# Performance work log

Measured on AMD Instinct MI355X. Metric: run time of the kernel, lower is better.

The kernel has to match this reference:

```python
import jax, jax.numpy as jnp
import numpy as np

B, N, C_IN, C_OUT, K = 8, 4096, 64, 128, 15
RADIUS = 0.1            # 2.5 * grid_size(0.04) * sigma(1.0)
MAX_NN = 34
KP_EXTENT = 0.04        # point_influence = prev_grid_size * sigma
KERNEL_RADIUS = 1.5 * KP_EXTENT
NEG_SLOPE = 0.2
BN_EPS = 1e-5


def setup_inputs() -> dict:
    key = jax.random.key(0)
    k1, k2, k3, k4 = jax.random.split(key, 4)
    xyz = jax.random.uniform(k1, (B, N, 3), dtype=jnp.float32)
    feats = jax.random.normal(k2, (B, N, C_IN), dtype=jnp.float32)
    # fixed kernel point disposition inside the kernel ball (requires_grad=False in torch)
    kp = jax.random.normal(k3, (K, 3), dtype=jnp.float32)
    kp = kp / (jnp.linalg.norm(kp, axis=-1, keepdims=True) + 1e-6) * KERNEL_RADIUS * 0.7
    kp = kp.at[0].set(0.0)  # center point
    std = float(np.sqrt(2.0 / (K * C_IN)))
    weight = jax.random.normal(k4, (K, C_IN, C_OUT), dtype=jnp.float32) * std
    gamma = jnp.ones((C_OUT,), dtype=jnp.float32)
    beta = jnp.zeros((C_OUT,), dtype=jnp.float32)
    return {"xyz": xyz, "feats": feats, "K_points": kp, "weight": weight,
            "gamma": gamma, "beta": beta}


def _ball_query(xyz):
    # xyz: [B, N, 3] -> flat neighbor idx [B*N, MAX_NN] into the concatenated
    # point array; missing neighbors get shadow index B*N.
    b_, n_, _ = xyz.shape
    shadow = b_ * n_

    def per_cloud(pts, b):
        d2 = jnp.sum((pts[:, None, :] - pts[None, :, :]) ** 2, axis=-1)  # [N, N]
        neg_d2, idx = jax.lax.top_k(-d2, MAX_NN)                         # k nearest
        valid = (-neg_d2) <= RADIUS ** 2
        return jnp.where(valid, idx + b * n_, shadow)

    return jax.vmap(per_cloud)(xyz, jnp.arange(b_)).reshape(b_ * n_, MAX_NN)


def _kpconv_block(xyz, feats, K_points, weight, gamma, beta):
    b_, n_, _ = xyz.shape
    pts = xyz.reshape(b_ * n_, 3)
    f = feats.reshape(b_ * n_, C_IN)
    nidx = _ball_query(xyz)                                   # [M, nn]
    # shadow point far away / zero features (KPConv_ops)
    pts_pad = jnp.concatenate([pts, jnp.full((1, 3), 1e6, pts.dtype)], axis=0)
    f_pad = jnp.concatenate([f, jnp.zeros((1, C_IN), f.dtype)], axis=0)
    nbr = pts_pad[nidx] - pts[:, None, :]                     # [M, nn, 3] relative coords
    sq = jnp.sum((nbr[:, :, None, :] - K_points) ** 2, -1)    # [M, nn, K]
    w = jnp.maximum(1.0 - jnp.sqrt(sq) / KP_EXTENT, 0.0)      # linear influence
    nf = f_pad[nidx]                                          # [M, nn, Cin]
    wf = jnp.einsum('mnk,mnc->mkc', w, nf)                    # per-kernel-point feats
    out = jnp.einsum('mkc,kcd->md', wf, weight)               # [M, Cout]
    # FastBatchNorm1d (training-mode batch stats, biased var) + LeakyReLU
    mu = out.mean(axis=0)
    var = out.var(axis=0)
    out = (out - mu) * jax.lax.rsqrt(var + BN_EPS) * gamma + beta
    out = jnp.where(out >= 0, out, NEG_SLOPE * out)
    return out.reshape(b_, n_, C_OUT)


def reference(xyz, feats, K_points, weight, gamma, beta):
    return _kpconv_block(xyz, feats, K_points, weight, gamma, beta)
```

## Files before the change

kernel.cpp:

```cpp
#include <hip/hip_runtime.h>


#define NB     8
#define NPTS   4096
#define M_TOT  32768
#define CIN    64
#define COUT   128
#define NKP    15
#define NCELL  1728
#define UCAP   400
#define R2EFF  (0.082f * 0.082f)
#define KP_INV 25.0f
#define NEG_SLOPE 0.2f
#define KCP    960
#define WFROW  1920
#define SP     40

typedef float f32x4_t __attribute__((ext_vector_type(4)));
typedef short bf16x8_t __attribute__((ext_vector_type(8)));

__device__ __forceinline__ unsigned short f2bf(float f) {
  union { float f; unsigned u; } v; v.f = f;
  unsigned r = v.u + 0x7FFF + ((v.u >> 16) & 1);
  return (unsigned short)(r >> 16);
}
__device__ __forceinline__ unsigned short f2bf_fast(float f) {
  union { float f; unsigned u; } v; v.f = f;
  return (unsigned short)((v.u + 0x8000u) >> 16);
}
__device__ __forceinline__ int cell_of(float x, float y, float z) {
  int cx = (int)(x * 12.f); cx = cx > 11 ? 11 : cx;
  int cy = (int)(y * 12.f); cy = cy > 11 ? 11 : cy;
  int cz = (int)(z * 12.f); cz = cz > 11 ? 11 : cz;
  return (cz * 12 + cy) * 12 + cx;
}

__global__ __launch_bounds__(256) void k0a_hist(
    const float* __restrict__ xyz, int* __restrict__ cellcnt)
{
  const int pt = blockIdx.x * 256 + threadIdx.x;
  const float x = xyz[pt * 3], y = xyz[pt * 3 + 1], z = xyz[pt * 3 + 2];
  const int b = pt >> 12;
  atomicAdd(&cellcnt[b * NCELL + cell_of(x, y, z)], 1);
}

__global__ __launch_bounds__(256) void k0b_scan_kWF(
    const int* __restrict__ cellcnt, int* __restrict__ cellstart,
    const float* __restrict__ W, unsigned short* __restrict__ WtF)
{
  if (blockIdx.x >= 8) {
    const int idx = (blockIdx.x - 8) * 256 + threadIdx.x;
    const int L  = idx & 63;
    const int g  = idx >> 6;
    const int kk = g % 30;
    const int ct = g / 30;
    const int d  = ct * 16 + (L & 15);
    const int kcb = (L >> 4) * 8 + kk * 32;
    union { unsigned short s[8]; uint4 v; } u;
    #pragma unroll
    for (int e = 0; e < 8; e++) {
      const int kc = kcb + e;
      const int k  = kc >> 6;
      const int c  = kc & 63;
      u.s[e] = f2bf(W[(size_t)k * (CIN * COUT) + c * COUT + d]);
    }
    *(uint4*)&WtF[(size_t)idx * 8] = u.v;
    return;
  }
  __shared__ int ps[256];
  const int b = blockIdx.x, t = threadIdx.x;
  int local[7], s = 0;
  #pragma unroll
  for (int i = 0; i < 7; i++) {
    const int cid = t * 7 + i;
    const int c = (cid < NCELL) ? cellcnt[b * NCELL + cid] : 0;
    local[i] = c; s += c;
  }
  ps[t] = s; __syncthreads();
  for (int off = 1; off < 256; off <<= 1) {
    int v = (t >= off) ? ps[t - off] : 0;
    __syncthreads();
    ps[t] += v;
    __syncthreads();
  }
  int run = ps[t] - s;
  #pragma unroll
  for (int i = 0; i < 7; i++) {
    const int cid = t * 7 + i;
    if (cid < NCELL) { cellstart[b * 1729 + cid] = run; run += local[i]; }
  }
  if (t == 255) cellstart[b * 1729 + NCELL] = ps[255];
}

__global__ __launch_bounds__(256) void k0b_old(
    const int* __restrict__ cellcnt, int* __restrict__ cellstart,
    const float* __restrict__ W, unsigned short* __restrict__ Wt)
{
  if (blockIdx.x >= 8) {
    const int idx = (blockIdx.x - 8) * 256 + threadIdx.x;
    const int c = idx & 63, d = idx >> 6;
    #pragma unroll
    for (int k = 0; k < NKP; k++)
      Wt[(size_t)d * KCP + k * 64 + c] =
          f2bf(W[(size_t)k * (CIN * COUT) + c * COUT + d]);
    return;
  }
  __shared__ int ps[256];
  const int b = blockIdx.x, t = threadIdx.x;
  int local[7], s = 0;
  #pragma unroll
  for (int i = 0; i < 7; i++) {
    const int cid = t * 7 + i;
    const int c = (cid < NCELL) ? cellcnt[b * NCELL + cid] : 0;
    local[i] = c; s += c;
  }
  ps[t] = s; __syncthreads();
  for (int off = 1; off < 256; off <<= 1) {
    int v = (t >= off) ? ps[t - off] : 0;
    __syncthreads();
    ps[t] += v;
    __syncthreads();
  }
  int run = ps[t] - s;
  #pragma unroll
  for (int i = 0; i < 7; i++) {
    const int cid = t * 7 + i;
    if (cid < NCELL) { cellstart[b * 1729 + cid] = run; run += local[i]; }
  }
  if (t == 255) cellstart[b * 1729 + NCELL] = ps[255];
}

__global__ __launch_bounds__(256) void k0c_scatter(
    const float* __restrict__ xyz, const float* __restrict__ feats,
    const int* __restrict__ cellstart, int* __restrict__ cellfill,
    int* __restrict__ qorder, float4* __restrict__ xyzs,
    unsigned short* __restrict__ fsorted)
{
  const int pt = blockIdx.x * 256 + threadIdx.x;
  const float x = xyz[pt * 3], y = xyz[pt * 3 + 1], z = xyz[pt * 3 + 2];
  const int b = pt >> 12;
  const int cid = cell_of(x, y, z);
  const int slot = atomicAdd(&cellfill[b * NCELL + cid], 1);
  const int pos = b * NPTS + cellstart[b * 1729 + cid] + slot;
  qorder[pos] = pt;
  xyzs[pos] = make_float4(x, y, z, 0.f);
  const float* src = &feats[(size_t)pt * CIN];
  uint4* dst = (uint4*)&fsorted[(size_t)pos * CIN];
  #pragma unroll
  for (int g = 0; g < 8; g++) {
    float4 a = *(const float4*)(src + g * 8);
    float4 c = *(const float4*)(src + g * 8 + 4);
    union { unsigned short s[8]; uint4 v; } u;
    u.s[0] = f2bf(a.x); u.s[1] = f2bf(a.y); u.s[2] = f2bf(a.z); u.s[3] = f2bf(a.w);
    u.s[4] = f2bf(c.x); u.s[5] = f2bf(c.y); u.s[6] = f2bf(c.z); u.s[7] = f2bf(c.w);
    dst[g] = u.v;
  }
}

__global__ __launch_bounds__(256, 5) void k2a_conv(
    const float4* __restrict__ xyzs, const unsigned short* __restrict__ fsorted,
    const float* __restrict__ kpts, const int* __restrict__ cellstart,
    unsigned short* __restrict__ wfg)
{
  __shared__ char smraw[32000] __attribute__((aligned(16)));
  float4*         Pu   = (float4*)smraw;
  unsigned short* cpos = (unsigned short*)(smraw + 6400);
  short (*S)[SP]       = (short(*)[SP])(smraw + 6400);
  short (*FT)[SP]      = (short(*)[SP])(smraw + 26880);

  __shared__ float4 qd[16];
  __shared__ float  kp[NKP][4];
  __shared__ int    Tsh;
  __shared__ int    ucnt;

  const int tid = threadIdx.x;
  const int w   = tid >> 6;
  const int L   = tid & 63;
  const int m0  = blockIdx.x * 16;
  const int b   = m0 >> 12;

  if (tid >= 64 && tid < 64 + NKP) {
    const int k = tid - 64;
    const float kx = kpts[k * 3], ky = kpts[k * 3 + 1], kz = kpts[k * 3 + 2];
    kp[k][0] = -2.f * kx; kp[k][1] = -2.f * ky; kp[k][2] = -2.f * kz;
    kp[k][3] = kx * kx + ky * ky + kz * kz;
  }

  if (tid < 64) {
    int cxm = 12, cym = 12, czm = 12, cxM = -1, cyM = -1, czM = -1;
    if (tid < 16) {
      const float4 Q = xyzs[m0 + tid];
      qd[tid] = Q;
      int a = (int)(Q.x * 12.f); a = a > 11 ? 11 : a;
      int c = (int)(Q.y * 12.f); c = c > 11 ? 11 : c;
      int d = (int)(Q.z * 12.f); d = d > 11 ? 11 : d;
      cxm = cxM = a; cym = cyM = c; czm = czM = d;
    }
    #pragma unroll
    for (int off = 8; off >= 1; off >>= 1) {
      int v;
      v = __shfl_xor(cxm, off); cxm = v < cxm ? v : cxm;
      v = __shfl_xor(cxM, off); cxM = v > cxM ? v : cxM;
      v = __shfl_xor(cym, off); cym = v < cym ? v : cym;
      v = __shfl_xor(cyM, off); cyM = v > cyM ? v : cyM;
      v = __shfl_xor(czm, off); czm = v < czm ? v : czm;
      v = __shfl_xor(czM, off); czM = v > czM ? v : czM;
    }
    cxm = __shfl(cxm, 0); cxM = __shfl(cxM, 0);
    cym = __shfl(cym, 0); cyM = __shfl(cyM, 0);
    czm = __shfl(czm, 0); czM = __shfl(czM, 0);

    const int x0 = cxm > 0 ? cxm - 1 : 0, x1 = cxM < 11 ? cxM + 1 : 11;
    const int y0 = cym > 0 ? cym - 1 : 0, y1 = cyM < 11 ? cyM + 1 : 11;
    const int z0 = czm > 0 ? czm - 1 : 0, z1 = czM < 11 ? czM + 1 : 11;
    const int yspan = y1 - y0 + 1;
    int nr = yspan * (z1 - z0 + 1);
    nr = nr > 64 ? 64 : nr;

    int rs = 0, len = 0;
    if (tid < nr) {
      const int zz = z0 + tid / yspan, yy = y0 + tid % yspan;
      const int base = b * 1729 + (zz * 12 + yy) * 12;
      rs  = cellstart[base + x0];
      len = cellstart[base + x1 + 1] - rs;
    }
    int incl = len;
    #pragma unroll
    for (int off = 1; off < 64; off <<= 1) {
      const int v = __shfl_up(incl, off);
      if (tid >= off) incl += v;
    }
    const int excl = incl - len;
    for (int i = 0; i < len; i++) cpos[excl + i] = (unsigned short)(rs + i);
    if (tid == 63) Tsh = incl;
    if (tid == 62) ucnt = 0;
  }
  __syncthreads();
  const int T = Tsh;

  for (int tb = 0; tb < T; tb += 256) {
    const int t = tb + tid;
    if (t < T) {
      const int pos = (int)cpos[t];
      const float4 P = xyzs[b * NPTS + pos];
      float best = 1e9f;
      #pragma unroll
      for (int i = 0; i < 16; i++) {
        const float4 Q = qd[i];
        const float dx = P.x - Q.x, dy = P.y - Q.y, dz = P.z - Q.z;
        const float d2 = dx * dx + dy * dy + dz * dz;
        best = d2 < best ? d2 : best;
      }
      if (best <= R2EFF) {
        const int slot = atomicAdd(&ucnt, 1);
        if (slot < UCAP)
          Pu[slot] = make_float4(P.x, P.y, P.z, __int_as_float(pos));
      }
    }
  }
  __syncthreads();
  int U = ucnt; U = U > UCAP ? UCAP : U;

  const int ln = L & 15;
  const int kh = L >> 4;
  const int qh = tid >> 5;
  const int nn = tid & 31;

  f32x4_t acc[16];
  #pragma unroll
  for (int mt = 0; mt < 16; mt++) acc[mt] = (f32x4_t){0.f, 0.f, 0.f, 0.f};

  for (int ub = 0; ub < U; ub += 32) {
    {
      const int c  = tid & 63;
      const int i0 = tid >> 6;
      #pragma unroll
      for (int ii = 0; ii < 8; ii++) {
        const int i = ii * 4 + i0;
        const int u = ub + i;
        short v = 0;
        if (u < U) {
          const int pos = __float_as_int(Pu[u].w);
          v = (short)fsorted[(size_t)(b * NPTS + pos) * CIN + c];
        }
        FT[c][i] = v;
      }
    }

    bf16x8_t bb;
    #pragma unroll
    for (int half = 0; half < 2; half++) {
      {
        const int u = ub + nn;
        if (u < U) {
          const float4 P = Pu[u];
          const float4 Q = qd[half * 8 + qh];
          const float rx = P.x - Q.x, ry = P.y - Q.y, rz = P.z - Q.z;
          const float rr = rx * rx + ry * ry + rz * rz;
          #pragma unroll
          for (int k = 0; k < NKP; k++) {
            float d2 = fmaf(kp[k][0], rx,
                       fmaf(kp[k][1], ry,
                       fmaf(kp[k][2], rz, rr + kp[k][3])));
            d2 = fmaxf(d2, 0.f);
            const float wv =
                fmaxf(fmaf(-KP_INV, __builtin_amdgcn_sqrtf(d2), 1.f), 0.f);
            S[qh * 16 + k][nn] = (short)f2bf_fast(wv);
          }
          S[qh * 16 + 15][nn] = 0;
        } else {
          #pragma unroll
          for (int k = 0; k < 16; k++) S[qh * 16 + k][nn] = 0;
        }
      }
      __syncthreads();
      if (half == 0) bb = *(const bf16x8_t*)&FT[w * 16 + ln][kh * 8];
      #pragma unroll
      for (int mt = 0; mt < 8; mt++) {
        bf16x8_t aa = *(const bf16x8_t*)&S[mt * 16 + ln][kh * 8];
        acc[half * 8 + mt] =
            __builtin_amdgcn_mfma_f32_16x16x32_bf16(aa, bb, acc[half * 8 + mt],
                                                    0, 0, 0);
      }
      __syncthreads();
    }
  }

  #pragma unroll
  for (int mt = 0; mt < 16; mt++) {
    const size_t rb = (size_t)(m0 + mt) * KCP + (w * 16 + ln);
    #pragma unroll
    for (int j = 0; j < 4; j++) {
      const int k = kh * 4 + j;
      if (k < 15)
        wfg[rb + k * 64] = f2bf_fast(acc[mt][j]);
    }
  }
}

__global__ __launch_bounds__(256, 5) void k2b_gemm(
    const unsigned short* __restrict__ wfg,
    const unsigned short* __restrict__ WtF,
    const int* __restrict__ qorder, float* __restrict__ out,
    float* __restrict__ psum, float* __restrict__ psumsq)
{
  __shared__ char smraw[30720] __attribute__((aligned(16)));
  __shared__ int qm[16];

  const int tid = threadIdx.x;
  const int w   = tid >> 6;
  const int L   = tid & 63;
  const int m0  = blockIdx.x * 16;

  if (tid < 16) qm[tid] = qorder[m0 + tid];

  {
    const int r0 = tid >> 7;
    const int ch = tid & 127;
    if (ch < 120) {
      #pragma unroll
      for (int it = 0; it < 8; it++) {
        const int r = it * 2 + r0;
        const uint4 v = *(const uint4*)(wfg + (size_t)(m0 + r) * KCP + ch * 8);
        *(uint4*)(smraw + ((r * WFROW + ch * 16) ^ ((r & 7) << 4))) = v;
      }
    }
  }
  __syncthreads();

  const int ln = L & 15;
  const int kh = L >> 4;
  const int colbase = w * 32;

  f32x4_t acc2[2];
  acc2[0] = (f32x4_t){0.f, 0.f, 0.f, 0.f};
  acc2[1] = (f32x4_t){0.f, 0.f, 0.f, 0.f};

  const unsigned short* Bp = WtF + ((size_t)(w * 2 * 30) * 64 + L) * 8;
  const char* wfb = (const char*)smraw + ln * WFROW;
  const int   sw  = (ln & 7) << 4;

  #pragma unroll 6
  for (int kk = 0; kk < 30; kk++) {
    const int inr = (kh * 16 + kk * 64) ^ sw;
    bf16x8_t b0 = *(const bf16x8_t*)(Bp + kk * 512);
    bf16x8_t b1 = *(const bf16x8_t*)(Bp + 15360 + kk * 512);
    bf16x8_t a0 = *(const bf16x8_t*)(wfb + inr);
    acc2[0] = __builtin_amdgcn_mfma_f32_16x16x32_bf16(a0, b0, acc2[0], 0, 0, 0);
    acc2[1] = __builtin_amdgcn_mfma_f32_16x16x32_bf16(a0, b1, acc2[1], 0, 0, 0);
  }

  float s0 = 0.f, q0 = 0.f, s1 = 0.f, q1 = 0.f;
  #pragma unroll
  for (int j = 0; j < 4; j++) {
    s0 += acc2[0][j]; q0 += acc2[0][j] * acc2[0][j];
    s1 += acc2[1][j]; q1 += acc2[1][j] * acc2[1][j];
  }
  s0 += __shfl_xor(s0, 16); s0 += __shfl_xor(s0, 32);
  q0 += __shfl_xor(q0, 16); q0 += __shfl_xor(q0, 32);
  s1 += __shfl_xor(s1, 16); s1 += __shfl_xor(s1, 32);
  q1 += __shfl_xor(q1, 16); q1 += __shfl_xor(q1, 32);
  if (kh == 0) {
    atomicAdd(&psum[colbase + ln], s0);
    atomicAdd(&psumsq[colbase + ln], q0);
    atomicAdd(&psum[colbase + 16 + ln], s1);
    atomicAdd(&psumsq[colbase + 16 + ln], q1);
  }

  #pragma unroll
  for (int c = 0; c < 2; c++) {
    #pragma unroll
    for (int j = 0; j < 4; j++) {
      const int row = kh * 4 + j;
      out[(size_t)qm[row] * COUT + colbase + c * 16 + ln] = acc2[c][j];
    }
  }
}

__global__ __launch_bounds__(256, 5) void k2_old(
    const float4* __restrict__ xyzs, const unsigned short* __restrict__ fsorted,
    const float* __restrict__ kpts, const int* __restrict__ cellstart,
    const int* __restrict__ qorder, const unsigned short* __restrict__ Wt,
    float* __restrict__ out, float* __restrict__ psum,
    float* __restrict__ psumsq)
{
  __shared__ char smraw[32000] __attribute__((aligned(16)));
  float4*         Pu   = (float4*)smraw;
  unsigned short* cpos = (unsigned short*)(smraw + 6400);
  short (*S)[SP]       = (short(*)[SP])(smraw + 6400);
  short (*FT)[SP]      = (short(*)[SP])(smraw + 26880);

  __shared__ float4 qd[16];
  __shared__ int    qm[16];
  __shared__ float  kp[NKP][4];
  __shared__ int    Tsh;
  __shared__ int    ucnt;

  const int tid = threadIdx.x;
  const int w   = tid >> 6;
  const int L   = tid & 63;
  const int m0  = blockIdx.x * 16;
  const int b   = m0 >> 12;

  if (tid >= 64 && tid < 64 + NKP) {
    const int k = tid - 64;
    const float kx = kpts[k * 3], ky = kpts[k * 3 + 1], kz = kpts[k * 3 + 2];
    kp[k][0] = -2.f * kx; kp[k][1] = -2.f * ky; kp[k][2] = -2.f * kz;
    kp[k][3] = kx * kx + ky * ky + kz * kz;
  }

  if (tid < 64) {
    int cxm = 12, cym = 12, czm = 12, cxM = -1, cyM = -1, czM = -1;
    if (tid < 16) {
      const float4 Q = xyzs[m0 + tid];
      qd[tid] = Q;
      qm[tid] = qorder[m0 + tid];
      int a = (int)(Q.x * 12.f); a = a > 11 ? 11 : a;
      int c = (int)(Q.y * 12.f); c = c > 11 ? 11 : c;
      int d = (int)(Q.z * 12.f); d = d > 11 ? 11 : d;
      cxm = cxM = a; cym = cyM = c; czm = czM = d;
    }
    #pragma unroll
    for (int off = 8; off >= 1; off >>= 1) {
      int v;
      v = __shfl_xor(cxm, off); cxm = v < cxm ? v : cxm;
      v = __shfl_xor(cxM, off); cxM = v > cxM ? v : cxM;
      v = __shfl_xor(cym, off); cym = v < cym ? v : cym;
      v = __shfl_xor(cyM, off); cyM = v > cyM ? v : cyM;
      v = __shfl_xor(czm, off); czm = v < czm ? v : czm;
      v = __shfl_xor(czM, off); czM = v > czM ? v : czM;
    }
    cxm = __shfl(cxm, 0); cxM = __shfl(cxM, 0);
    cym = __shfl(cym, 0); cyM = __shfl(cyM, 0);
    czm = __shfl(czm, 0); czM = __shfl(czM, 0);

    const int x0 = cxm > 0 ? cxm - 1 : 0, x1 = cxM < 11 ? cxM + 1 : 11;
    const int y0 = cym > 0 ? cym - 1 : 0, y1 = cyM < 11 ? cyM + 1 : 11;
    const int z0 = czm > 0 ? czm - 1 : 0, z1 = czM < 11 ? czM + 1 : 11;
    const int yspan = y1 - y0 + 1;
    int nr = yspan * (z1 - z0 + 1);
    nr = nr > 64 ? 64 : nr;

    int rs = 0, len = 0;
    if (tid < nr) {
      const int zz = z0 + tid / yspan, yy = y0 + tid % yspan;
      const int base = b * 1729 + (zz * 12 + yy) * 12;
      rs  = cellstart[base + x0];
      len = cellstart[base + x1 + 1] - rs;
    }
    int incl = len;
    #pragma unroll
    for (int off = 1; off < 64; off <<= 1) {
      const int v = __shfl_up(incl, off);
      if (tid >= off) incl += v;
    }
    const int excl = incl - len;
    for (int i = 0; i < len; i++) cpos[excl + i] = (unsigned short)(rs + i);
    if (tid == 63) Tsh = incl;
    if (tid == 62) ucnt = 0;
  }
  __syncthreads();
  const int T = Tsh;

  for (int tb = 0; tb < T; tb += 256) {
    const int t = tb + tid;
    if (t < T) {
      const int pos = (int)cpos[t];
      const float4 P = xyzs[b * NPTS + pos];
      float best = 1e9f;
      #pragma unroll
      for (int i = 0; i < 16; i++) {
        const float4 Q = qd[i];
        const float dx = P.x - Q.x, dy = P.y - Q.y, dz = P.z - Q.z;
        const float d2 = dx * dx + dy * dy + dz * dz;
        best = d2 < best ? d2 : best;
      }
      if (best <= R2EFF) {
        const int slot = atomicAdd(&ucnt, 1);
        if (slot < UCAP)
          Pu[slot] = make_float4(P.x, P.y, P.z, __int_as_float(pos));
      }
    }
  }
  __syncthreads();
  int U = ucnt; U = U > UCAP ? UCAP : U;

  const int ln = L & 15;
  const int kh = L >> 4;
  const int qh = tid >> 5;
  const int nn = tid & 31;

  f32x4_t acc[16];
  #pragma unroll
  for (int mt = 0; mt < 16; mt++) acc[mt] = (f32x4_t){0.f, 0.f, 0.f, 0.f};

  for (int ub = 0; ub < U; ub += 32) {
    {
      const int c  = tid & 63;
      const int i0 = tid >> 6;
      #pragma unroll
      for (int ii = 0; ii < 8; ii++) {
        const int i = ii * 4 + i0;
        const int u = ub + i;
        short v = 0;
        if (u < U) {
          const int pos = __float_as_int(Pu[u].w);
          v = (short)fsorted[(size_t)(b * NPTS + pos) * CIN + c];
        }
        FT[c][i] = v;
      }
    }
    bf16x8_t bb;
    #pragma unroll
    for (int half = 0; half < 2; half++) {
      {
        const int u = ub + nn;
        if (u < U) {
          const float4 P = Pu[u];
          const float4 Q = qd[half * 8 + qh];
          const float rx = P.x - Q.x, ry = P.y - Q.y, rz = P.z - Q.z;
          const float rr = rx * rx + ry * ry + rz * rz;
          #pragma unroll
          for (int k = 0; k < NKP; k++) {
            float d2 = fmaf(kp[k][0], rx,
                       fmaf(kp[k][1], ry,
                       fmaf(kp[k][2], rz, rr + kp[k][3])));
            d2 = fmaxf(d2, 0.f);
            const float wv =
                fmaxf(fmaf(-KP_INV, __builtin_amdgcn_sqrtf(d2), 1.f), 0.f);
            S[qh * 16 + k][nn] = (short)f2bf_fast(wv);
          }
          S[qh * 16 + 15][nn] = 0;
        } else {
          #pragma unroll
          for (int k = 0; k < 16; k++) S[qh * 16 + k][nn] = 0;
        }
      }
      __syncthreads();
      if (half == 0) bb = *(const bf16x8_t*)&FT[w * 16 + ln][kh * 8];
      #pragma unroll
      for (int mt = 0; mt < 8; mt++) {
        bf16x8_t aa = *(const bf16x8_t*)&S[mt * 16 + ln][kh * 8];
        acc[half * 8 + mt] =
            __builtin_amdgcn_mfma_f32_16x16x32_bf16(aa, bb, acc[half * 8 + mt],
                                                    0, 0, 0);
      }
      __syncthreads();
    }
  }

  {
    const int c = w * 16 + ln;
    #pragma unroll
    for (int mt = 0; mt < 16; mt++) {
      #pragma unroll
      for (int j = 0; j < 4; j++) {
        const int k = kh * 4 + j;
        if (k < 15) {
          const int byteo = (mt * WFROW + ((k * 64 + c) << 1)) ^ ((mt & 7) << 4);
          *(unsigned short*)(smraw + byteo) = f2bf_fast(acc[mt][j]);
        }
      }
    }
  }
  __syncthreads();

  const int colbase = w * 32;
  f32x4_t acc2[2];
  acc2[0] = (f32x4_t){0.f, 0.f, 0.f, 0.f};
  acc2[1] = (f32x4_t){0.f, 0.f, 0.f, 0.f};

  const unsigned short* Bp0 = &Wt[(size_t)(colbase + ln) * KCP + kh * 8];
  const unsigned short* Bp1 = Bp0 + 16 * KCP;
  const char* wfb = (const char*)smraw + ln * WFROW;
  const int   sw  = (ln & 7) << 4;

  #pragma unroll 6
  for (int kk = 0; kk < 30; kk++) {
    const int ko  = kk * 32;
    const int inr = (kh * 16 + kk * 64) ^ sw;
    bf16x8_t b0 = *(const bf16x8_t*)(Bp0 + ko);
    bf16x8_t b1 = *(const bf16x8_t*)(Bp1 + ko);
    bf16x8_t a0 = *(const bf16x8_t*)(wfb + inr);
    acc2[0] = __builtin_amdgcn_mfma_f32_16x16x32_bf16(a0, b0, acc2[0], 0, 0, 0);
    acc2[1] = __builtin_amdgcn_mfma_f32_16x16x32_bf16(a0, b1, acc2[1], 0, 0, 0);
  }

  float s0 = 0.f, q0 = 0.f, s1 = 0.f, q1 = 0.f;
  #pragma unroll
  for (int j = 0; j < 4; j++) {
    s0 += acc2[0][j]; q0 += acc2[0][j] * acc2[0][j];
    s1 += acc2[1][j]; q1 += acc2[1][j] * acc2[1][j];
  }
  s0 += __shfl_xor(s0, 16); s0 += __shfl_xor(s0, 32);
  q0 += __shfl_xor(q0, 16); q0 += __shfl_xor(q0, 32);
  s1 += __shfl_xor(s1, 16); s1 += __shfl_xor(s1, 32);
  q1 += __shfl_xor(q1, 16); q1 += __shfl_xor(q1, 32);
  if (kh == 0) {
    atomicAdd(&psum[colbase + ln], s0);
    atomicAdd(&psumsq[colbase + ln], q0);
    atomicAdd(&psum[colbase + 16 + ln], s1);
    atomicAdd(&psumsq[colbase + 16 + ln], q1);
  }

  #pragma unroll
  for (int c = 0; c < 2; c++) {
    #pragma unroll
    for (int j = 0; j < 4; j++) {
      const int row = kh * 4 + j;
      out[(size_t)qm[row] * COUT + colbase + c * 16 + ln] = acc2[c][j];
    }
  }
}

__global__ __launch_bounds__(256) void k4_norm(
    float* __restrict__ out, const float* __restrict__ psum,
    const float* __restrict__ psumsq, const float* __restrict__ gamma,
    const float* __restrict__ beta)
{
  __shared__ float a_s[128], b_s[128];
  if (threadIdx.x < 128) {
    const int d = threadIdx.x;
    double mu  = (double)psum[d] / (double)M_TOT;
    double var = (double)psumsq[d] / (double)M_TOT - mu * mu;
    float rstd = (float)(1.0 / sqrt(var + 1e-5));
    float a = rstd * gamma[d];
    a_s[d] = a;
    b_s[d] = beta[d] - (float)mu * a;
  }
  __syncthreads();
  const int idx = blockIdx.x * 256 + threadIdx.x;
  float4 v = ((const float4*)out)[idx];
  const int d0 = (idx * 4) & 127;
  float y0 = v.x * a_s[d0 + 0] + b_s[d0 + 0];
  float y1 = v.y * a_s[d0 + 1] + b_s[d0 + 1];
  float y2 = v.z * a_s[d0 + 2] + b_s[d0 + 2];
  float y3 = v.w * a_s[d0 + 3] + b_s[d0 + 3];
  v.x = y0 >= 0.f ? y0 : NEG_SLOPE * y0;
  v.y = y1 >= 0.f ? y1 : NEG_SLOPE * y1;
  v.z = y2 >= 0.f ? y2 : NEG_SLOPE * y2;
  v.w = y3 >= 0.f ? y3 : NEG_SLOPE * y3;
  ((float4*)out)[idx] = v;
}

extern "C" void kernel_launch(void* const* d_in, const int* in_sizes, int n_in,
                              void* d_out, int out_size, void* d_ws,
                              size_t ws_size, hipStream_t stream)
{
  const float* xyz   = (const float*)d_in[0];
  const float* feats = (const float*)d_in[1];
  const float* kpts  = (const float*)d_in[2];
  const float* W     = (const float*)d_in[3];
  const float* gamma = (const float*)d_in[4];
  const float* beta  = (const float*)d_in[5];
  float* out = (float*)d_out;

  char* ws = (char*)d_ws;
  int*            cellcnt   = (int*)(ws + 0);
  int*            cellfill  = (int*)(ws + 55296);
  float*          psum      = (float*)(ws + 110592);
  float*          psumsq    = (float*)(ws + 111104);
  int*            cellstart = (int*)(ws + 111616);
  int*            qorder    = (int*)(ws + 167040);
  float4*         xyzs      = (float4*)(ws + 298112);
  unsigned short* fsorted   = (unsigned short*)(ws + 822400);
  unsigned short* Wtbuf     = (unsigned short*)(ws + 5016704);
  unsigned short* wfg       = (unsigned short*)(ws + 5262464);

  const size_t NEED = 5262464ull + 62914560ull;

  hipMemsetAsync(ws, 0, 111616, stream);

  if (ws_size >= NEED) {
    k0a_hist    <<< 128, 256, 0, stream>>>(xyz, cellcnt);
    k0b_scan_kWF<<<  68, 256, 0, stream>>>(cellcnt, cellstart, W, Wtbuf);
    k0c_scatter <<< 128, 256, 0, stream>>>(xyz, feats, cellstart, cellfill,
                                           qorder, xyzs, fsorted);
    k2a_conv    <<<2048, 256, 0, stream>>>(xyzs, fsorted, kpts, cellstart,
                                           wfg);
    k2b_gemm    <<<2048, 256, 0, stream>>>(wfg, Wtbuf, qorder, out,
                                           psum, psumsq);
    k4_norm     <<<(out_size / 4) / 256, 256, 0, stream>>>(out, psum, psumsq,
                                                           gamma, beta);
  } else {
    k0a_hist    <<< 128, 256, 0, stream>>>(xyz, cellcnt);
    k0b_old     <<<  40, 256, 0, stream>>>(cellcnt, cellstart, W, Wtbuf);
    k0c_scatter <<< 128, 256, 0, stream>>>(xyz, feats, cellstart, cellfill,
                                           qorder, xyzs, fsorted);
    k2_old      <<<2048, 256, 0, stream>>>(xyzs, fsorted, kpts, cellstart,
                                           qorder, Wtbuf, out, psum, psumsq);
    k4_norm     <<<(out_size / 4) / 256, 256, 0, stream>>>(out, psum, psumsq,
                                                           gamma, beta);
  }
}
```

Before: 205.3 us.

## Retile GEMM stage to 128x128 blocks with double-buffered direct-to-LDS loads

The second-stage GEMM moves from 16-row blocks, which read a pre-swizzled weight layout straight from global memory, to 128x128 output tiles. Each of 4 waves computes a 64x64 sub-tile, and A/B k-slices are staged into swizzled LDS through global_load_lds with double buffering. The weight prep goes back to the plain [d][k*64+c] transpose kernel. This raises reuse of weight and activation tiles per block, but leaves only 256 blocks with fewer waves per CU and more accumulator registers.

New measurement: 174.2 us. -15.1%, faster.

```diff
diff --git a/kernel.cpp b/kernel.cpp
--- a/kernel.cpp
+++ b/kernel.cpp
@@ -34,6 +34,11 @@
   int cz = (int)(z * 12.f); cz = cz > 11 ? 11 : cz;
   return (cz * 12 + cy) * 12 + cx;
 }
+__device__ __forceinline__ void gld_lds16(const unsigned short* g, void* l) {
+  __builtin_amdgcn_global_load_lds(
+      (const __attribute__((address_space(1))) unsigned int*)g,
+      (__attribute__((address_space(3))) unsigned int*)l, 16, 0, 0);
+}
 
 __global__ __launch_bounds__(256) void k0a_hist(
     const float* __restrict__ xyz, int* __restrict__ cellcnt)
@@ -44,55 +49,7 @@
   atomicAdd(&cellcnt[b * NCELL + cell_of(x, y, z)], 1);
 }
 
-__global__ __launch_bounds__(256) void k0b_scan_kWF(
-    const int* __restrict__ cellcnt, int* __restrict__ cellstart,
-    const float* __restrict__ W, unsigned short* __restrict__ WtF)
-{
-  if (blockIdx.x >= 8) {
-    const int idx = (blockIdx.x - 8) * 256 + threadIdx.x;
-    const int L  = idx & 63;
-    const int g  = idx >> 6;
-    const int kk = g % 30;
-    const int ct = g / 30;
-    const int d  = ct * 16 + (L & 15);
-    const int kcb = (L >> 4) * 8 + kk * 32;
-    union { unsigned short s[8]; uint4 v; } u;
-    #pragma unroll
-    for (int e = 0; e < 8; e++) {
-      const int kc = kcb + e;
-      const int k  = kc >> 6;
-      const int c  = kc & 63;
-      u.s[e] = f2bf(W[(size_t)k * (CIN * COUT) + c * COUT + d]);
-    }
-    *(uint4*)&WtF[(size_t)idx * 8] = u.v;
-    return;
-  }
-  __shared__ int ps[256];
-  const int b = blockIdx.x, t = threadIdx.x;
-  int local[7], s = 0;
-  #pragma unroll
-  for (int i = 0; i < 7; i++) {
-    const int cid = t * 7 + i;
-    const int c = (cid < NCELL) ? cellcnt[b * NCELL + cid] : 0;
-    local[i] = c; s += c;
-  }
-  ps[t] = s; __syncthreads();
-  for (int off = 1; off < 256; off <<= 1) {
-    int v = (t >= off) ? ps[t - off] : 0;
-    __syncthreads();
-    ps[t] += v;
-    __syncthreads();
-  }
-  int run = ps[t] - s;
-  #pragma unroll
-  for (int i = 0; i < 7; i++) {
-    const int cid = t * 7 + i;
-    if (cid < NCELL) { cellstart[b * 1729 + cid] = run; run += local[i]; }
-  }
-  if (t == 255) cellstart[b * 1729 + NCELL] = ps[255];
-}
-
-__global__ __launch_bounds__(256) void k0b_old(
+__global__ __launch_bounds__(256) void k0b_scan_kW(
     const int* __restrict__ cellcnt, int* __restrict__ cellstart,
     const float* __restrict__ W, unsigned short* __restrict__ Wt)
 {
@@ -338,81 +295,111 @@
   }
 }
 
-__global__ __launch_bounds__(256, 5) void k2b_gemm(
+__global__ __launch_bounds__(256, 2) void k2b_gemm(
     const unsigned short* __restrict__ wfg,
-    const unsigned short* __restrict__ WtF,
+    const unsigned short* __restrict__ Wt,
     const int* __restrict__ qorder, float* __restrict__ out,
     float* __restrict__ psum, float* __restrict__ psumsq)
 {
-  __shared__ char smraw[30720] __attribute__((aligned(16)));
-  __shared__ int qm[16];
+  __shared__ char smA[2][16384] __attribute__((aligned(16)));
+  __shared__ char smB[2][16384] __attribute__((aligned(16)));
+  __shared__ int  qm[128];
 
   const int tid = threadIdx.x;
   const int w   = tid >> 6;
   const int L   = tid & 63;
-  const int m0  = blockIdx.x * 16;
-
-  if (tid < 16) qm[tid] = qorder[m0 + tid];
-
-  {
-    const int r0 = tid >> 7;
-    const int ch = tid & 127;
-    if (ch < 120) {
-      #pragma unroll
-      for (int it = 0; it < 8; it++) {
-        const int r = it * 2 + r0;
-        const uint4 v = *(const uint4*)(wfg + (size_t)(m0 + r) * KCP + ch * 8);
-        *(uint4*)(smraw + ((r * WFROW + ch * 16) ^ ((r & 7) << 4))) = v;
-      }
-    }
-  }
+  const int m0  = blockIdx.x * 128;
+
+  if (tid < 128) qm[tid] = qorder[m0 + tid];
+
+  const int c16 = L & 7;
+
+#define STAGE_TILES(buf, ks)                                                 \
+  {                                                                          \
+    _Pragma("unroll")                                                        \
+    for (int i = 0; i < 4; i++) {                                            \
+      const int row = (w * 4 + i) * 8 + (L >> 3);                            \
+      const int sc  = (c16 ^ (row & 7)) << 3;                    \
+      gld_lds16(wfg + (size_t)(m0 + row) * KCP + (ks) * 64 + sc,             \
+                (char*)smA[buf] + (w * 4 + i) * 1024);                       \
+      gld_lds16(Wt + (size_t)row * KCP + (ks) * 64 + sc,                     \
+                (char*)smB[buf] + (w * 4 + i) * 1024);                       \
+    }                                                                        \
+  }
+
+  STAGE_TILES(0, 0)
   __syncthreads();
 
-  const int ln = L & 15;
-  const int kh = L >> 4;
-  const int colbase = w * 32;
-
-  f32x4_t acc2[2];
-  acc2[0] = (f32x4_t){0.f, 0.f, 0.f, 0.f};
-  acc2[1] = (f32x4_t){0.f, 0.f, 0.f, 0.f};
-
-  const unsigned short* Bp = WtF + ((size_t)(w * 2 * 30) * 64 + L) * 8;
-  const char* wfb = (const char*)smraw + ln * WFROW;
-  const int   sw  = (ln & 7) << 4;
-
-  #pragma unroll 6
-  for (int kk = 0; kk < 30; kk++) {
-    const int inr = (kh * 16 + kk * 64) ^ sw;
-    bf16x8_t b0 = *(const bf16x8_t*)(Bp + kk * 512);
-    bf16x8_t b1 = *(const bf16x8_t*)(Bp + 15360 + kk * 512);
-    bf16x8_t a0 = *(const bf16x8_t*)(wfb + inr);
-    acc2[0] = __builtin_amdgcn_mfma_f32_16x16x32_bf16(a0, b0, acc2[0], 0, 0, 0);
-    acc2[1] = __builtin_amdgcn_mfma_f32_16x16x32_bf16(a0, b1, acc2[1], 0, 0, 0);
-  }
-
-  float s0 = 0.f, q0 = 0.f, s1 = 0.f, q1 = 0.f;
-  #pragma unroll
-  for (int j = 0; j < 4; j++) {
-    s0 += acc2[0][j]; q0 += acc2[0][j] * acc2[0][j];
-    s1 += acc2[1][j]; q1 += acc2[1][j] * acc2[1][j];
-  }
-  s0 += __shfl_xor(s0, 16); s0 += __shfl_xor(s0, 32);
-  q0 += __shfl_xor(q0, 16); q0 += __shfl_xor(q0, 32);
-  s1 += __shfl_xor(s1, 16); s1 += __shfl_xor(s1, 32);
-  q1 += __shfl_xor(q1, 16); q1 += __shfl_xor(q1, 32);
-  if (kh == 0) {
-    atomicAdd(&psum[colbase + ln], s0);
-    atomicAdd(&psumsq[colbase + ln], q0);
-    atomicAdd(&psum[colbase + 16 + ln], s1);
-    atomicAdd(&psumsq[colbase + 16 + ln], q1);
-  }
-
-  #pragma unroll
-  for (int c = 0; c < 2; c++) {
+  const int wr = w >> 1, wc = w & 1;
+  const int ln = L & 15, kh = L >> 4;
+
+  f32x4_t acc[4][4];
+  #pragma unroll
+  for (int mt = 0; mt < 4; mt++)
+    #pragma unroll
+    for (int nt = 0; nt < 4; nt++)
+      acc[mt][nt] = (f32x4_t){0.f, 0.f, 0.f, 0.f};
+
+  int cur = 0;
+  for (int ks = 0; ks < 15; ks++) {
+    if (ks < 14) STAGE_TILES(cur ^ 1, ks + 1)
+
+    const char* cA = smA[cur];
+    const char* cB = smB[cur];
+    #pragma unroll
+    for (int ks2 = 0; ks2 < 2; ks2++) {
+      bf16x8_t a[4], bfr[4];
+      #pragma unroll
+      for (int mt = 0; mt < 4; mt++) {
+        const int row  = wr * 64 + mt * 16 + ln;
+        const int phys = ((ks2 * 4 + kh) ^ (row & 7)) << 4;
+        a[mt] = *(const bf16x8_t*)(cA + row * 128 + phys);
+      }
+      #pragma unroll
+      for (int nt = 0; nt < 4; nt++) {
+        const int row  = wc * 64 + nt * 16 + ln;
+        const int phys = ((ks2 * 4 + kh) ^ (row & 7)) << 4;
+        bfr[nt] = *(const bf16x8_t*)(cB + row * 128 + phys);
+      }
+      #pragma unroll
+      for (int mt = 0; mt < 4; mt++)
+        #pragma unroll
+        for (int nt = 0; nt < 4; nt++)
+          acc[mt][nt] = __builtin_amdgcn_mfma_f32_16x16x32_bf16(
+              a[mt], bfr[nt], acc[mt][nt], 0, 0, 0);
+    }
+    __syncthreads();
+    cur ^= 1;
+  }
+#undef STAGE_TILES
+
+  #pragma unroll
+  for (int nt = 0; nt < 4; nt++) {
+    float s = 0.f, q = 0.f;
+    #pragma unroll
+    for (int mt = 0; mt < 4; mt++)
+      #pragma unroll
+      for (int j = 0; j < 4; j++) {
+        const float v = acc[mt][nt][j];
+        s += v; q += v * v;
+      }
+    s += __shfl_xor(s, 16); s += __shfl_xor(s, 32);
+    q += __shfl_xor(q, 16); q += __shfl_xor(q, 32);
+    if (kh == 0) {
+      atomicAdd(&psum[wc * 64 + nt * 16 + ln], s);
+      atomicAdd(&psumsq[wc * 64 + nt * 16 + ln], q);
+    }
+  }
+
+  #pragma unroll
+  for (int mt = 0; mt < 4; mt++) {
     #pragma unroll
     for (int j = 0; j < 4; j++) {
-      const int row = kh * 4 + j;
-      out[(size_t)qm[row] * COUT + colbase + c * 16 + ln] = acc2[c][j];
+      const int r = wr * 64 + mt * 16 + kh * 4 + j;
+      const size_t ob = (size_t)qm[r] * COUT + wc * 64 + ln;
+      #pragma unroll
+      for (int nt = 0; nt < 4; nt++)
+        out[ob + nt * 16] = acc[mt][nt][j];
     }
   }
 }
@@ -713,18 +700,18 @@
 
   if (ws_size >= NEED) {
     k0a_hist    <<< 128, 256, 0, stream>>>(xyz, cellcnt);
-    k0b_scan_kWF<<<  68, 256, 0, stream>>>(cellcnt, cellstart, W, Wtbuf);
+    k0b_scan_kW <<<  40, 256, 0, stream>>>(cellcnt, cellstart, W, Wtbuf);
     k0c_scatter <<< 128, 256, 0, stream>>>(xyz, feats, cellstart, cellfill,
                                            qorder, xyzs, fsorted);
     k2a_conv    <<<2048, 256, 0, stream>>>(xyzs, fsorted, kpts, cellstart,
                                            wfg);
-    k2b_gemm    <<<2048, 256, 0, stream>>>(wfg, Wtbuf, qorder, out,
+    k2b_gemm    <<< 256, 256, 0, stream>>>(wfg, Wtbuf, qorder, out,
                                            psum, psumsq);
     k4_norm     <<<(out_size / 4) / 256, 256, 0, stream>>>(out, psum, psumsq,
                                                            gamma, beta);
   } else {
     k0a_hist    <<< 128, 256, 0, stream>>>(xyz, cellcnt);
-    k0b_old     <<<  40, 256, 0, stream>>>(cellcnt, cellstart, W, Wtbuf);
+    k0b_scan_kW <<<  40, 256, 0, stream>>>(cellcnt, cellstart, W, Wtbuf);
     k0c_scatter <<< 128, 256, 0, stream>>>(xyz, feats, cellstart, cellfill,
                                            qorder, xyzs, fsorted);
     k2_old      <<<2048, 256, 0, stream>>>(xyzs, fsorted, kpts, cellstart,
```
